# Performance work log

Measured on AMD Instinct MI355X. Metric: run time of the kernel, lower is better.

The kernel has to match this reference:

```python
import jax, jax.numpy as jnp
import numpy as np

EPS = 1e-4


def setup_inputs() -> dict:
    key = jax.random.key(0)
    ks = jax.random.split(key, 9)
    B, N, OBS, PRED, IN, E, C, K = 2048, 64, 8, 12, 6, 512, 6, 20
    d_self = IN * (OBS + PRED)  # 120
    d_nei = IN * OBS            # 48
    obs = jax.random.normal(ks[0], (B, OBS, IN), dtype=jnp.float32)
    neis = jax.random.normal(ks[1], (B, N, OBS, IN), dtype=jnp.float32)
    self_labels = jax.random.randint(ks[2], (B,), 0, C)
    nei_labels = jax.random.randint(ks[3], (B, N), 0, C + 1)
    init_trajs = jax.random.normal(ks[4], (C, K, PRED, IN), dtype=jnp.float32)
    # per-class Linear params, stored [in, out] (torch Linear is x @ W.T + b)
    W_self = jax.random.normal(ks[5], (C, d_self, E), dtype=jnp.float32) * (1.0 / np.sqrt(d_self))
    b_self = jax.random.normal(ks[6], (C, E), dtype=jnp.float32) * 0.02
    W_nei = jax.random.normal(ks[7], (C + 1, d_nei, E), dtype=jnp.float32) * (1.0 / np.sqrt(d_nei))
    b_nei = jax.random.normal(ks[8], (C + 1, E), dtype=jnp.float32) * 0.02
    return {"obs": obs, "neis": neis, "init_trajs": init_trajs,
            "W_self": W_self, "b_self": b_self, "W_nei": W_nei, "b_nei": b_nei,
            "self_labels": self_labels, "nei_labels": nei_labels}


def reference(obs, neis, init_trajs, W_self, b_self, W_nei, b_nei, self_labels, nei_labels):
    B = obs.shape[0]
    N = neis.shape[1]
    C, _, E = W_self.shape
    Cn = W_nei.shape[0]  # num_class + 1

    # gather per-sample anchor trajectories: [B, K, pred_len, in_size]
    it = init_trajs[self_labels]
    K = it.shape[1]
    obs_r = jnp.broadcast_to(obs[:, None], (B, K) + obs.shape[1:])
    traj = jnp.concatenate([obs_r, it], axis=2).reshape(B, K, -1)  # [B, K, in*(obs+pred)]

    # label-conditioned self embedding: loop over small fixed class count
    x = jnp.zeros((B, K, E), dtype=traj.dtype)
    for c in range(C):
        out_c = traj @ W_self[c] + b_self[c]
        x = jnp.where((self_labels == c)[:, None, None], out_c, x)

    # elementwise signed-reciprocal transform on neighbor features
    neis_f = neis.reshape(B, N, -1)  # [B, N, in*obs]
    neis_t = jnp.where(neis_f >= 0, 1.0 / (neis_f + EPS), 1.0 / (neis_f - EPS))

    # label-conditioned neighbor embedding over num_class+1 classes
    nei_feats = jnp.zeros((B, N, E), dtype=neis_t.dtype)
    for c in range(Cn):
        out_c = neis_t @ W_nei[c] + b_nei[c]
        nei_feats = jnp.where((nei_labels == c)[:, :, None], out_c, nei_feats)

    return x, nei_feats
```

## Files before the change

kernel.cpp:

```cpp
#include <hip/hip_runtime.h>

#define B_    2048
#define N_    64
#define E_    512
#define K_    20
#define C_    6
#define DSELF 120
#define DNEI  48
#define DPRED 72
#define EPS_  1e-4f

#define C2_ELEMS ((size_t)C_ * K_ * E_)
#define NT_ELEMS ((size_t)B_ * N_ * DNEI)
#define WS_NEED  ((C2_ELEMS + NT_ELEMS) * sizeof(float))

#define TBLOCKS 1536

__global__ __launch_bounds__(256) void prep(
    const float* __restrict__ neis,
    const float* __restrict__ init_trajs,
    const float* __restrict__ W_self,
    const float* __restrict__ b_self,
    float*       __restrict__ ws)
{
    const int tid = threadIdx.x;
    const int bid = blockIdx.x;
    if (bid < C_ * K_) {
        const int c = bid / K_;
        const float* itr = init_trajs + (size_t)bid * DPRED;
        const float2* Wp = reinterpret_cast<const float2*>(
                               W_self + ((size_t)c * DSELF + DNEI) * E_) + tid;
        float2 acc = reinterpret_cast<const float2*>(b_self + (size_t)c * E_)[tid];
        #pragma unroll
        for (int j = 0; j < DPRED; ++j) {
            const float t  = itr[j];
            const float2 w = Wp[(size_t)j * (E_ / 2)];
            acc.x += t * w.x; acc.y += t * w.y;
        }
        reinterpret_cast<float2*>(ws + (size_t)bid * E_)[tid] = acc;
    } else {
        const int ib = bid - C_ * K_;
        const size_t base   = (size_t)ib * 256 + tid;
        const size_t stride = (size_t)TBLOCKS * 256;
        const float4* in4 = reinterpret_cast<const float4*>(neis);
        float4* o4 = reinterpret_cast<float4*>(ws + C2_ELEMS);
        #pragma unroll
        for (int t = 0; t < 4; ++t) {
            const size_t idx = base + (size_t)t * stride;
            const float4 v = in4[idx];
            float4 o;
            o.x = (v.x >= 0.f) ? 1.f / (v.x + EPS_) : 1.f / (v.x - EPS_);
            o.y = (v.y >= 0.f) ? 1.f / (v.y + EPS_) : 1.f / (v.y - EPS_);
            o.z = (v.z >= 0.f) ? 1.f / (v.z + EPS_) : 1.f / (v.z - EPS_);
            o.w = (v.w >= 0.f) ? 1.f / (v.w + EPS_) : 1.f / (v.w - EPS_);
            o4[idx] = o;
        }
    }
}

__global__ __launch_bounds__(256) void self_fast(
    const float* __restrict__ obs,
    const float* __restrict__ W_self,
    const int*   __restrict__ labels,
    const float* __restrict__ c2,
    float*       __restrict__ out)
{
    const int b   = blockIdx.x;
    const int tid = threadIdx.x;
    const int c   = labels[b];

    const float*  ob = obs + (size_t)b * DNEI;
    const float2* Wp = reinterpret_cast<const float2*>(
                           W_self + (size_t)c * DSELF * E_) + tid;
    float ax = 0.f, ay = 0.f;
    #pragma unroll
    for (int j = 0; j < DNEI; ++j) {
        const float t  = ob[j];
        const float2 w = Wp[(size_t)j * (E_ / 2)];
        ax += t * w.x; ay += t * w.y;
    }

    const float2* cp = reinterpret_cast<const float2*>(
                           c2 + (size_t)c * K_ * E_) + tid;
    float2* op = reinterpret_cast<float2*>(out + (size_t)b * K_ * E_) + tid;
    #pragma unroll
    for (int k = 0; k < K_; ++k) {
        const float2 v = cp[(size_t)k * (E_ / 2)];
        float2 o; o.x = ax + v.x; o.y = ay + v.y;
        op[(size_t)k * (E_ / 2)] = o;
    }
}

__global__ __launch_bounds__(256) void nei_gemm(
    const float* __restrict__ nts,
    const float* __restrict__ W_nei,
    const float* __restrict__ b_nei,
    const int*   __restrict__ labels,
    float*       __restrict__ out)
{
    const int b   = blockIdx.x;
    const int tid = threadIdx.x;

    __shared__ int lab[N_];
    if (tid < N_) lab[tid] = labels[b * N_ + tid];
    __syncthreads();

    float wl[DNEI], wh[DNEI];

    for (int c = 0; c < C_ + 1; ++c) {
        const float2* Wp = reinterpret_cast<const float2*>(
                               W_nei + (size_t)c * DNEI * E_) + tid;
        #pragma unroll
        for (int j = 0; j < DNEI; ++j) {
            const float2 w = Wp[(size_t)j * (E_ / 2)];
            wl[j] = w.x;
            wh[j] = w.y;
        }
        const float2 bs = reinterpret_cast<const float2*>(
                              b_nei + (size_t)c * E_)[tid];

        for (int n = 0; n < N_; ++n) {
            if (lab[n] != c) continue;
            const float* r = nts + ((size_t)b * N_ + n) * DNEI;
            float a0 = bs.x, a1 = bs.y;
            #pragma unroll
            for (int j = 0; j < DNEI; ++j) {
                const float t = r[j];
                a0 += t * wl[j];
                a1 += t * wh[j];
            }
            float2 o; o.x = a0; o.y = a1;
            reinterpret_cast<float2*>(out + ((size_t)b * N_ + n) * E_)[tid] = o;
        }
    }
}

__global__ __launch_bounds__(256) void self_embed_fb(
    const float* __restrict__ obs,
    const float* __restrict__ init_trajs,
    const float* __restrict__ W_self,
    const float* __restrict__ b_self,
    const int*   __restrict__ labels,
    float*       __restrict__ out)
{
    const int b   = blockIdx.x;
    const int tid = threadIdx.x;
    const int c   = labels[b];

    __shared__ __align__(16) float traj[DSELF * K_];

    for (int idx = tid; idx < DSELF * K_; idx += 256) {
        const int j = idx / K_;
        const int k = idx - j * K_;
        float v;
        if (j < DNEI) v = obs[b * DNEI + j];
        else          v = init_trajs[(c * K_ + k) * DPRED + (j - DNEI)];
        traj[idx] = v;
    }
    __syncthreads();

    float acc[K_][2];
    #pragma unroll
    for (int k = 0; k < K_; ++k) { acc[k][0] = 0.f; acc[k][1] = 0.f; }

    const float2* Wp = reinterpret_cast<const float2*>(W_self + (size_t)c * DSELF * E_) + tid;

    for (int j = 0; j < DSELF; ++j) {
        const float2 w  = Wp[j * (E_ / 2)];
        const float4* tp = reinterpret_cast<const float4*>(&traj[j * K_]);
        #pragma unroll
        for (int q = 0; q < 5; ++q) {
            const float4 t4 = tp[q];
            acc[q * 4 + 0][0] += t4.x * w.x; acc[q * 4 + 0][1] += t4.x * w.y;
            acc[q * 4 + 1][0] += t4.y * w.x; acc[q * 4 + 1][1] += t4.y * w.y;
            acc[q * 4 + 2][0] += t4.z * w.x; acc[q * 4 + 2][1] += t4.z * w.y;
            acc[q * 4 + 3][0] += t4.w * w.x; acc[q * 4 + 3][1] += t4.w * w.y;
        }
    }

    const float2 bs = reinterpret_cast<const float2*>(b_self + c * E_)[tid];
    #pragma unroll
    for (int k = 0; k < K_; ++k) {
        float2 o;
        o.x = acc[k][0] + bs.x;
        o.y = acc[k][1] + bs.y;
        reinterpret_cast<float2*>(out + (size_t)(b * K_ + k) * E_)[tid] = o;
    }
}

__global__ __launch_bounds__(256) void nei_embed_fb(
    const float* __restrict__ neis,
    const float* __restrict__ W_nei,
    const float* __restrict__ b_nei,
    const int*   __restrict__ labels,
    float*       __restrict__ out)
{
    const int b   = blockIdx.x;
    const int tid = threadIdx.x;

    __shared__ __align__(16) float nt[N_ * DNEI];
    __shared__ int lab[N_];

    if (tid < N_) lab[tid] = labels[b * N_ + tid];

    const float4* np4 = reinterpret_cast<const float4*>(neis + (size_t)b * N_ * DNEI);
    float4* nt4 = reinterpret_cast<float4*>(nt);
    #pragma unroll
    for (int i = 0; i < 3; ++i) {
        const int idx = tid + i * 256;
        float4 v = np4[idx];
        float4 o;
        o.x = (v.x >= 0.f) ? 1.f / (v.x + EPS_) : 1.f / (v.x - EPS_);
        o.y = (v.y >= 0.f) ? 1.f / (v.y + EPS_) : 1.f / (v.y - EPS_);
        o.z = (v.z >= 0.f) ? 1.f / (v.z + EPS_) : 1.f / (v.z - EPS_);
        o.w = (v.w >= 0.f) ? 1.f / (v.w + EPS_) : 1.f / (v.w - EPS_);
        nt4[idx] = o;
    }
    __syncthreads();

    float wl[DNEI], wh[DNEI];

    for (int c = 0; c < C_ + 1; ++c) {
        const float2* Wp = reinterpret_cast<const float2*>(W_nei + (size_t)c * DNEI * E_) + tid;
        #pragma unroll
        for (int j = 0; j < DNEI; ++j) {
            const float2 w = Wp[j * (E_ / 2)];
            wl[j] = w.x;
            wh[j] = w.y;
        }
        const float2 bs = reinterpret_cast<const float2*>(b_nei + c * E_)[tid];

        for (int n = 0; n < N_; ++n) {
            if (lab[n] != c) continue;
            float a0 = bs.x, a1 = bs.y;
            const float4* tp = reinterpret_cast<const float4*>(&nt[n * DNEI]);
            #pragma unroll
            for (int q = 0; q < 12; ++q) {
                const float4 t4 = tp[q];
                a0 += t4.x * wl[q * 4 + 0]; a1 += t4.x * wh[q * 4 + 0];
                a0 += t4.y * wl[q * 4 + 1]; a1 += t4.y * wh[q * 4 + 1];
                a0 += t4.z * wl[q * 4 + 2]; a1 += t4.z * wh[q * 4 + 2];
                a0 += t4.w * wl[q * 4 + 3]; a1 += t4.w * wh[q * 4 + 3];
            }
            float2 o; o.x = a0; o.y = a1;
            reinterpret_cast<float2*>(out + (size_t)(b * N_ + n) * E_)[tid] = o;
        }
    }
}

extern "C" void kernel_launch(void* const* d_in, const int* in_sizes, int n_in,
                              void* d_out, int out_size, void* d_ws, size_t ws_size,
                              hipStream_t stream) {
    const float* obs  = (const float*)d_in[0];
    const float* neis = (const float*)d_in[1];
    const float* it   = (const float*)d_in[2];
    const float* Ws   = (const float*)d_in[3];
    const float* bs   = (const float*)d_in[4];
    const float* Wn   = (const float*)d_in[5];
    const float* bn   = (const float*)d_in[6];
    const int* sl = (const int*)d_in[7];
    const int* nl = (const int*)d_in[8];

    float* out_x = (float*)d_out;
    float* out_n = out_x + (size_t)B_ * K_ * E_;

    if (d_ws != nullptr && ws_size >= WS_NEED) {
        float* c2 = (float*)d_ws;
        float* nt = c2 + C2_ELEMS;
        prep<<<dim3(C_ * K_ + TBLOCKS), dim3(256), 0, stream>>>(neis, it, Ws, bs, (float*)d_ws);
        self_fast<<<dim3(B_), dim3(256), 0, stream>>>(obs, Ws, sl, c2, out_x);
        nei_gemm<<<dim3(B_), dim3(256), 0, stream>>>(nt, Wn, bn, nl, out_n);
    } else {
        self_embed_fb<<<dim3(B_), dim3(256), 0, stream>>>(obs, it, Ws, bs, sl, out_x);
        nei_embed_fb<<<dim3(B_), dim3(256), 0, stream>>>(neis, Wn, bn, nl, out_n);
    }
}
```

Measured before the change: 617.8 us.

## Fuse neighbor reciprocal transform into GEMM via register-held rows and readlane broadcast

```diff
diff --git a/kernel.cpp b/kernel.cpp
--- a/kernel.cpp
+++ b/kernel.cpp
@@ -11,51 +11,28 @@
 #define EPS_  1e-4f
 
 #define C2_ELEMS ((size_t)C_ * K_ * E_)
-#define NT_ELEMS ((size_t)B_ * N_ * DNEI)
-#define WS_NEED  ((C2_ELEMS + NT_ELEMS) * sizeof(float))
-
-#define TBLOCKS 1536
+#define WS_NEED  (C2_ELEMS * sizeof(float))
 
 __global__ __launch_bounds__(256) void prep(
-    const float* __restrict__ neis,
     const float* __restrict__ init_trajs,
     const float* __restrict__ W_self,
     const float* __restrict__ b_self,
-    float*       __restrict__ ws)
+    float*       __restrict__ c2)
 {
     const int tid = threadIdx.x;
     const int bid = blockIdx.x;
-    if (bid < C_ * K_) {
-        const int c = bid / K_;
-        const float* itr = init_trajs + (size_t)bid * DPRED;
-        const float2* Wp = reinterpret_cast<const float2*>(
-                               W_self + ((size_t)c * DSELF + DNEI) * E_) + tid;
-        float2 acc = reinterpret_cast<const float2*>(b_self + (size_t)c * E_)[tid];
-        #pragma unroll
-        for (int j = 0; j < DPRED; ++j) {
-            const float t  = itr[j];
-            const float2 w = Wp[(size_t)j * (E_ / 2)];
-            acc.x += t * w.x; acc.y += t * w.y;
-        }
-        reinterpret_cast<float2*>(ws + (size_t)bid * E_)[tid] = acc;
-    } else {
-        const int ib = bid - C_ * K_;
-        const size_t base   = (size_t)ib * 256 + tid;
-        const size_t stride = (size_t)TBLOCKS * 256;
-        const float4* in4 = reinterpret_cast<const float4*>(neis);
-        float4* o4 = reinterpret_cast<float4*>(ws + C2_ELEMS);
-        #pragma unroll
-        for (int t = 0; t < 4; ++t) {
-            const size_t idx = base + (size_t)t * stride;
-            const float4 v = in4[idx];
-            float4 o;
-            o.x = (v.x >= 0.f) ? 1.f / (v.x + EPS_) : 1.f / (v.x - EPS_);
-            o.y = (v.y >= 0.f) ? 1.f / (v.y + EPS_) : 1.f / (v.y - EPS_);
-            o.z = (v.z >= 0.f) ? 1.f / (v.z + EPS_) : 1.f / (v.z - EPS_);
-            o.w = (v.w >= 0.f) ? 1.f / (v.w + EPS_) : 1.f / (v.w - EPS_);
-            o4[idx] = o;
-        }
-    }
+    const int c = bid / K_;
+    const float* itr = init_trajs + (size_t)bid * DPRED;
+    const float2* Wp = reinterpret_cast<const float2*>(
+                           W_self + ((size_t)c * DSELF + DNEI) * E_) + tid;
+    float2 acc = reinterpret_cast<const float2*>(b_self + (size_t)c * E_)[tid];
+    #pragma unroll
+    for (int j = 0; j < DPRED; ++j) {
+        const float t  = itr[j];
+        const float2 w = Wp[(size_t)j * (E_ / 2)];
+        acc.x += t * w.x; acc.y += t * w.y;
+    }
+    reinterpret_cast<float2*>(c2 + (size_t)bid * E_)[tid] = acc;
 }
 
 __global__ __launch_bounds__(256) void self_fast(
@@ -91,19 +68,31 @@
     }
 }
 
-__global__ __launch_bounds__(256) void nei_gemm(
-    const float* __restrict__ nts,
+__global__ __launch_bounds__(256, 2) void nei_rl(
+    const float* __restrict__ neis,
     const float* __restrict__ W_nei,
     const float* __restrict__ b_nei,
     const int*   __restrict__ labels,
     float*       __restrict__ out)
 {
-    const int b   = blockIdx.x;
-    const int tid = threadIdx.x;
-
-    __shared__ int lab[N_];
-    if (tid < N_) lab[tid] = labels[b * N_ + tid];
-    __syncthreads();
+    const int b    = blockIdx.x;
+    const int tid  = threadIdx.x;
+    const int lane = tid & 63;
+
+    float r[DNEI];
+    {
+        const float4* src = reinterpret_cast<const float4*>(
+                                neis + (size_t)b * N_ * DNEI);
+        #pragma unroll
+        for (int i = 0; i < DNEI / 4; ++i) {
+            const float4 v = src[lane * (DNEI / 4) + i];
+            r[i * 4 + 0] = (v.x >= 0.f) ? 1.f / (v.x + EPS_) : 1.f / (v.x - EPS_);
+            r[i * 4 + 1] = (v.y >= 0.f) ? 1.f / (v.y + EPS_) : 1.f / (v.y - EPS_);
+            r[i * 4 + 2] = (v.z >= 0.f) ? 1.f / (v.z + EPS_) : 1.f / (v.z - EPS_);
+            r[i * 4 + 3] = (v.w >= 0.f) ? 1.f / (v.w + EPS_) : 1.f / (v.w - EPS_);
+        }
+    }
+    const int myLab = labels[b * N_ + lane];
 
     float wl[DNEI], wh[DNEI];
 
@@ -120,16 +109,20 @@
                               b_nei + (size_t)c * E_)[tid];
 
         for (int n = 0; n < N_; ++n) {
-            if (lab[n] != c) continue;
-            const float* r = nts + ((size_t)b * N_ + n) * DNEI;
-            float a0 = bs.x, a1 = bs.y;
+            const int labn = __builtin_amdgcn_readlane(myLab, n);
+            if (labn != c) continue;
+
+            float a0 = bs.x, a1 = bs.y, a2 = 0.f, a3 = 0.f;
             #pragma unroll
-            for (int j = 0; j < DNEI; ++j) {
-                const float t = r[j];
-                a0 += t * wl[j];
-                a1 += t * wh[j];
+            for (int j = 0; j < DNEI; j += 2) {
+                const float t0 = __int_as_float(
+                    __builtin_amdgcn_readlane(__float_as_int(r[j]), n));
+                const float t1 = __int_as_float(
+                    __builtin_amdgcn_readlane(__float_as_int(r[j + 1]), n));
+                a0 += t0 * wl[j];     a1 += t0 * wh[j];
+                a2 += t1 * wl[j + 1]; a3 += t1 * wh[j + 1];
             }
-            float2 o; o.x = a0; o.y = a1;
+            float2 o; o.x = a0 + a2; o.y = a1 + a3;
             reinterpret_cast<float2*>(out + ((size_t)b * N_ + n) * E_)[tid] = o;
         }
     }
@@ -185,66 +178,6 @@
         o.x = acc[k][0] + bs.x;
         o.y = acc[k][1] + bs.y;
         reinterpret_cast<float2*>(out + (size_t)(b * K_ + k) * E_)[tid] = o;
-    }
-}
-
-__global__ __launch_bounds__(256) void nei_embed_fb(
-    const float* __restrict__ neis,
-    const float* __restrict__ W_nei,
-    const float* __restrict__ b_nei,
-    const int*   __restrict__ labels,
-    float*       __restrict__ out)
-{
-    const int b   = blockIdx.x;
-    const int tid = threadIdx.x;
-
-    __shared__ __align__(16) float nt[N_ * DNEI];
-    __shared__ int lab[N_];
-
-    if (tid < N_) lab[tid] = labels[b * N_ + tid];
-
-    const float4* np4 = reinterpret_cast<const float4*>(neis + (size_t)b * N_ * DNEI);
-    float4* nt4 = reinterpret_cast<float4*>(nt);
-    #pragma unroll
-    for (int i = 0; i < 3; ++i) {
-        const int idx = tid + i * 256;
-        float4 v = np4[idx];
-        float4 o;
-        o.x = (v.x >= 0.f) ? 1.f / (v.x + EPS_) : 1.f / (v.x - EPS_);
-        o.y = (v.y >= 0.f) ? 1.f / (v.y + EPS_) : 1.f / (v.y - EPS_);
-        o.z = (v.z >= 0.f) ? 1.f / (v.z + EPS_) : 1.f / (v.z - EPS_);
-        o.w = (v.w >= 0.f) ? 1.f / (v.w + EPS_) : 1.f / (v.w - EPS_);
-        nt4[idx] = o;
-    }
-    __syncthreads();
-
-    float wl[DNEI], wh[DNEI];
-
-    for (int c = 0; c < C_ + 1; ++c) {
-        const float2* Wp = reinterpret_cast<const float2*>(W_nei + (size_t)c * DNEI * E_) + tid;
-        #pragma unroll
-        for (int j = 0; j < DNEI; ++j) {
-            const float2 w = Wp[j * (E_ / 2)];
-            wl[j] = w.x;
-            wh[j] = w.y;
-        }
-        const float2 bs = reinterpret_cast<const float2*>(b_nei + c * E_)[tid];
-
-        for (int n = 0; n < N_; ++n) {
-            if (lab[n] != c) continue;
-            float a0 = bs.x, a1 = bs.y;
-            const float4* tp = reinterpret_cast<const float4*>(&nt[n * DNEI]);
-            #pragma unroll
-            for (int q = 0; q < 12; ++q) {
-                const float4 t4 = tp[q];
-                a0 += t4.x * wl[q * 4 + 0]; a1 += t4.x * wh[q * 4 + 0];
-                a0 += t4.y * wl[q * 4 + 1]; a1 += t4.y * wh[q * 4 + 1];
-                a0 += t4.z * wl[q * 4 + 2]; a1 += t4.z * wh[q * 4 + 2];
-                a0 += t4.w * wl[q * 4 + 3]; a1 += t4.w * wh[q * 4 + 3];
-            }
-            float2 o; o.x = a0; o.y = a1;
-            reinterpret_cast<float2*>(out + (size_t)(b * N_ + n) * E_)[tid] = o;
-        }
     }
 }
 
@@ -264,14 +197,13 @@
     float* out_x = (float*)d_out;
     float* out_n = out_x + (size_t)B_ * K_ * E_;
 
+    nei_rl<<<dim3(B_), dim3(256), 0, stream>>>(neis, Wn, bn, nl, out_n);
+
     if (d_ws != nullptr && ws_size >= WS_NEED) {
         float* c2 = (float*)d_ws;
-        float* nt = c2 + C2_ELEMS;
-        prep<<<dim3(C_ * K_ + TBLOCKS), dim3(256), 0, stream>>>(neis, it, Ws, bs, (float*)d_ws);
+        prep<<<dim3(C_ * K_), dim3(256), 0, stream>>>(it, Ws, bs, c2);
         self_fast<<<dim3(B_), dim3(256), 0, stream>>>(obs, Ws, sl, c2, out_x);
-        nei_gemm<<<dim3(B_), dim3(256), 0, stream>>>(nt, Wn, bn, nl, out_n);
     } else {
         self_embed_fb<<<dim3(B_), dim3(256), 0, stream>>>(obs, it, Ws, bs, sl, out_x);
-        nei_embed_fb<<<dim3(B_), dim3(256), 0, stream>>>(neis, Wn, bn, nl, out_n);
-    }
-}
+    }
+}
```

Result: faster. 570.0 us (-7.7%).
